# Kernel optimization log

Hardware: AMD Instinct MI355X
Metric: run time of the kernel (lower is better)

## Reference

```python
import jax, jax.numpy as jnp
import numpy as np

N = 100000       # nodes
E = 1600000      # edges
NFEAT, NHID, NCLASS = 512, 256, 40
NLAYERS = 10     # APPNP propagation steps K
ALPHA = 0.1      # teleport probability


def setup_inputs() -> dict:
    key = jax.random.key(0)
    ks = jax.random.split(key, 8)
    x = jax.random.normal(ks[0], (N, NFEAT), jnp.float32)
    row = jax.random.randint(ks[1], (E,), 0, N, jnp.int32)
    col = jax.random.randint(ks[2], (E,), 0, N, jnp.int32)
    vals = jax.random.uniform(ks[3], (E,), jnp.float32)
    # MyLinear init: uniform(-stdv, stdv) with stdv = 1/sqrt(in_features);
    # bias is a shape-[1] scalar (faithful to torch.FloatTensor([out_features])).
    s1 = 1.0 / np.sqrt(NFEAT)
    s2 = 1.0 / np.sqrt(NHID)
    W1 = jax.random.uniform(ks[4], (NFEAT, NHID), jnp.float32, -s1, s1)
    b1 = jax.random.uniform(ks[5], (1,), jnp.float32, -s1, s1)
    W2 = jax.random.uniform(ks[6], (NHID, NCLASS), jnp.float32, -s2, s2)
    b2 = jax.random.uniform(ks[7], (1,), jnp.float32, -s2, s2)
    return dict(x=x, row=row, col=col, vals=vals, W1=W1, b1=b1, W2=W2, b2=b2)


def reference(x, row, col, vals, W1, b1, W2, b2):
    # 2-layer MLP (eval mode: dropout inactive, no BN)
    h = jax.nn.relu(x @ W1 + b1)          # [N, NHID]
    h = h @ W2 + b2                        # [N, NCLASS]

    # sparse adjacency spmm via edge-list segment sum
    def spmm(z):
        return jax.ops.segment_sum(vals[:, None] * z[col], row, num_segments=N)

    # APPNP propagation: z <- (1-alpha) * A z + alpha * h
    def step(z, _):
        z = (1.0 - ALPHA) * spmm(z) + ALPHA * h
        return z, None

    z, _ = jax.lax.scan(step, h, None, length=NLAYERS)
    return jax.nn.log_softmax(z, axis=1)
```

## Files before the change

### kernel.cpp

```cpp
#include <hip/hip_runtime.h>


typedef unsigned short ushort_t;
typedef short short8 __attribute__((ext_vector_type(8)));
typedef float f32x4 __attribute__((ext_vector_type(4)));

#define NFEAT 512
#define NHID 256
#define NCLASS 40

static __device__ __forceinline__ float b2f(ushort_t u) {
    unsigned v = ((unsigned)u) << 16;
    float f;
    __builtin_memcpy(&f, &v, 4);
    return f;
}
static __device__ __forceinline__ ushort_t f2b(float f) {
    unsigned u;
    __builtin_memcpy(&u, &f, 4);
    unsigned r = u + 0x7FFFu + ((u >> 16) & 1u);
    return (ushort_t)(r >> 16);
}
static __device__ __forceinline__ ushort_t san_u(ushort_t u) {
    return ((u & 0x7F80u) == 0x7F80u) ? (ushort_t)0 : u;
}
static __device__ __forceinline__ float ldmix(const void* p, size_t i, int isbf) {
    if (isbf) return b2f(san_u(((const ushort_t*)p)[i]));
    return ((const float*)p)[i];
}
static __device__ __forceinline__ float ldz(const void* p, size_t i, int zbf) {
    return zbf ? b2f(((const ushort_t*)p)[i]) : ((const float*)p)[i];
}
static __device__ __forceinline__ void stz(void* p, size_t i, int zbf, float v) {
    if (zbf) ((ushort_t*)p)[i] = f2b(v);
    else ((float*)p)[i] = v;
}

static __device__ __forceinline__ void gld_lds16(const ushort_t* g, ushort_t* l) {
    __builtin_amdgcn_global_load_lds(
        (const __attribute__((address_space(1))) unsigned int*)g,
        (__attribute__((address_space(3))) unsigned int*)l, 16, 0, 0);
}

__global__ void detect_kernel(const ushort_t* __restrict__ x, int* __restrict__ flag) {
    __shared__ int cnt_s;
    if (threadIdx.x == 0) cnt_s = 0;
    __syncthreads();
    int c = 0;
    for (int i = threadIdx.x; i < 2048; i += 256) {
        ushort_t u = x[2 * i];
        int e = (u >> 7) & 0xFF;
        if (e >= 107 && e <= 141) c++;
    }
    atomicAdd(&cnt_s, c);
    __syncthreads();
    if (threadIdx.x == 0) flag[0] = (cnt_s >= 1024) ? 1 : 0;
}


__global__ void zero_kernel(int* __restrict__ p, int n) {
    int i = blockIdx.x * 256 + threadIdx.x;
    if (i < n) p[i] = 0;
}

__global__ void hist_kernel(const int* __restrict__ row, int* __restrict__ deg, int e, int n) {
    int i = blockIdx.x * 256 + threadIdx.x;
    if (i < e) {
        int r = row[i];
        if ((unsigned)r < (unsigned)n) atomicAdd(&deg[r], 1);
    }
}

__global__ void scan_blocksum(const int* __restrict__ deg, int* __restrict__ bsum, int n) {
    __shared__ int s[256];
    int t = threadIdx.x;
    int i = blockIdx.x * 256 + t;
    s[t] = (i < n) ? deg[i] : 0;
    __syncthreads();
    for (int o = 128; o; o >>= 1) {
        if (t < o) s[t] += s[t + o];
        __syncthreads();
    }
    if (t == 0) bsum[blockIdx.x] = s[0];
}

__global__ void scan_bsum_excl(int* __restrict__ bsum, int nb) {
    __shared__ int s[512];
    int t = threadIdx.x;
    int v = (t < nb) ? bsum[t] : 0;
    int own = v;
    s[t] = v;
    __syncthreads();
    for (int o = 1; o < 512; o <<= 1) {
        int add = (t >= o) ? s[t - o] : 0;
        __syncthreads();
        s[t] += add;
        __syncthreads();
    }
    if (t < nb) bsum[t] = s[t] - own;
}

__global__ void scan_emit(const int* __restrict__ deg, const int* __restrict__ bsum,
                          int* __restrict__ row_start, int* __restrict__ cursor, int n) {
    __shared__ int s[256];
    int t = threadIdx.x;
    int i = blockIdx.x * 256 + t;
    int v = (i < n) ? deg[i] : 0;
    int own = v;
    s[t] = v;
    __syncthreads();
    for (int o = 1; o < 256; o <<= 1) {
        int add = (t >= o) ? s[t - o] : 0;
        __syncthreads();
        s[t] += add;
        __syncthreads();
    }
    if (i < n) {
        int rs = bsum[blockIdx.x] + s[t] - own;
        row_start[i] = rs;
        cursor[i] = rs;
    }
}

__global__ void scatter_kernel(const int* __restrict__ row, const int* __restrict__ col,
                               const void* __restrict__ vals, int* __restrict__ cursor,
                               int* __restrict__ cs_col, void* __restrict__ cs_val,
                               const int* __restrict__ flag, int zbf, int e, int n) {
    int i = blockIdx.x * 256 + threadIdx.x;
    if (i < e) {
        int isbf = flag[0];
        int r = row[i];
        if ((unsigned)r >= (unsigned)n) return;
        int p = atomicAdd(&cursor[r], 1);
        if ((unsigned)p < (unsigned)e) {
            int c = col[i];
            cs_col[p] = ((unsigned)c < (unsigned)n) ? c : 0;
            stz(cs_val, p, zbf, ldmix(vals, i, isbf));
        }
    }
}


__global__ void w1frag_kernel(const void* __restrict__ W1, ushort_t* __restrict__ w1f,
                              const int* __restrict__ flag) {
    int t = blockIdx.x * 256 + threadIdx.x;
    if (t >= 16 * 16 * 64) return;
    int isbf = flag[0];
    int l = t & 63, nt = (t >> 6) & 15, kb = t >> 10;
    ushort_t tmp[8];
#pragma unroll
    for (int j = 0; j < 8; j++) {
        int k = kb * 32 + (l >> 4) * 8 + j;
        int nn = nt * 16 + (l & 15);
        tmp[j] = f2b(ldmix(W1, (size_t)k * NHID + nn, isbf));
    }
    *(short8*)(w1f + (size_t)t * 8) = *(short8*)tmp;
}

__global__ void w2frag_kernel(const void* __restrict__ W2, ushort_t* __restrict__ w2f,
                              const int* __restrict__ flag) {
    int t = blockIdx.x * 256 + threadIdx.x;
    if (t >= 8 * 3 * 64) return;
    int isbf = flag[0];
    int l = t % 64;
    int nt = (t / 64) % 3;
    int kb = t / 192;
    ushort_t tmp[8];
#pragma unroll
    for (int j = 0; j < 8; j++) {
        int k = kb * 32 + (l >> 4) * 8 + j;
        int nn = nt * 16 + (l & 15);
        tmp[j] = (nn < NCLASS) ? f2b(ldmix(W2, (size_t)k * NCLASS + nn, isbf)) : (ushort_t)0;
    }
    *(short8*)(w2f + (size_t)t * 8) = *(short8*)tmp;
}


template <int ISBF>
static __device__ __forceinline__ short8 load_afrag(const void* __restrict__ x, size_t base) {
    short8 av;
    if (ISBF) {
        av = *(const short8*)((const ushort_t*)x + base);
#pragma unroll
        for (int j = 0; j < 8; j++) {
            ushort_t u = (ushort_t)av[j];
            if ((u & 0x7F80u) == 0x7F80u) av[j] = 0;
        }
    } else {
        const float* xf = (const float*)x + base;
        f32x4 a0 = *(const f32x4*)xf;
        f32x4 a1 = *(const f32x4*)(xf + 4);
#pragma unroll
        for (int j = 0; j < 4; j++) {
            av[j] = (short)f2b(a0[j]);
            av[4 + j] = (short)f2b(a1[j]);
        }
    }
    return av;
}

#define APITCH 42

template <int ISBF>
static __device__ __forceinline__ void gemm1_staged(const void* __restrict__ x,
                                                    const ushort_t* __restrict__ w1f,
                                                    size_t xbase, ushort_t* Bl0, ushort_t* Bl1,
                                                    ushort_t* awr0, ushort_t* awr1,
                                                    const ushort_t* ard0, const ushort_t* ard1,
                                                    const ushort_t* brd0, const ushort_t* brd1,
                                                    f32x4 (&acc)[16], int wv, int l) {
    {
        short8 a0 = load_afrag<ISBF>(x, xbase);
        *(short8*)awr0 = a0;
        const ushort_t* src = w1f + (size_t)wv * 512 + (size_t)l * 8;
#pragma unroll
        for (int i = 0; i < 4; i++) gld_lds16(src + i * 2048, Bl0 + wv * 512 + i * 2048);
    }
    __syncthreads();

#pragma unroll
    for (int kb = 0; kb < 16; kb++) {
        const bool even = (kb & 1) == 0;
        const ushort_t* brd = even ? brd0 : brd1;
        const ushort_t* ard = even ? ard0 : ard1;
        ushort_t* awrn = even ? awr1 : awr0;
        ushort_t* bln = even ? Bl1 : Bl0;
        short8 an;
        if (kb < 15) {
            an = load_afrag<ISBF>(x, xbase + (size_t)(kb + 1) * 32);
            const ushort_t* src =
                w1f + (size_t)(kb + 1) * 8192 + (size_t)wv * 512 + (size_t)l * 8;
#pragma unroll
            for (int i = 0; i < 4; i++) gld_lds16(src + i * 2048, bln + wv * 512 + i * 2048);
        }
        short8 af = *(const short8*)ard;
#pragma unroll
        for (int nt = 0; nt < 16; nt++) {
            short8 bf = *(const short8*)(brd + nt * 512);
            acc[nt] = __builtin_amdgcn_mfma_f32_16x16x32_bf16(af, bf, acc[nt], 0, 0, 0);
        }
        if (kb < 15) *(short8*)awrn = an;
        __syncthreads();
    }
}

__global__ __launch_bounds__(256, 3) void mlp_kernel(const void* __restrict__ x,
                                                     const ushort_t* __restrict__ w1f,
                                                     const ushort_t* __restrict__ w2f,
                                                     const void* __restrict__ b1,
                                                     const void* __restrict__ b2,
                                                     void* __restrict__ h,
                                                     const int* __restrict__ flag, int zbf,
                                                     int n) {
    __shared__ __align__(16) ushort_t pool[21760];
    ushort_t* Bl0 = pool;
    ushort_t* Bl1 = pool + 8192;
    ushort_t* Al0 = pool + 16384;
    ushort_t* Al1 = pool + 16384 + 2688;
    ushort_t* Hl = pool;

    const int t = threadIdx.x;
    const int isbf = flag[0];
    const int wv = t >> 6, l = t & 63;
    const int lq = l >> 4, lr = l & 15;
    const int m0 = blockIdx.x * 64;

    const int rS = t >> 2, qS = t & 3;
    int rowS = m0 + rS;
    if (rowS > n - 1) rowS = n - 1;
    const size_t xbase = (size_t)rowS * NFEAT + (size_t)qS * 8;
    ushort_t* awr0 = Al0 + rS * APITCH + qS * 8;
    ushort_t* awr1 = Al1 + rS * APITCH + qS * 8;
    const ushort_t* ard0 = Al0 + (wv * 16 + lr) * APITCH + lq * 8;
    const ushort_t* ard1 = Al1 + (wv * 16 + lr) * APITCH + lq * 8;
    const ushort_t* brd0 = Bl0 + l * 8;
    const ushort_t* brd1 = Bl1 + l * 8;

    f32x4 acc[16];
#pragma unroll
    for (int i = 0; i < 16; i++) acc[i] = (f32x4){0.f, 0.f, 0.f, 0.f};

    if (isbf)
        gemm1_staged<1>(x, w1f, xbase, Bl0, Bl1, awr0, awr1, ard0, ard1, brd0, brd1, acc, wv, l);
    else
        gemm1_staged<0>(x, w1f, xbase, Bl0, Bl1, awr0, awr1, ard0, ard1, brd0, brd1, acc, wv, l);

    float bias1 = ldmix(b1, 0, isbf);
#pragma unroll
    for (int nt = 0; nt < 16; nt++) {
#pragma unroll
        for (int i = 0; i < 4; i++) {
            float v = acc[nt][i] + bias1;
            v = fmaxf(v, 0.f);
            Hl[(wv * 16 + lq * 4 + i) * 264 + nt * 16 + lr] = f2b(v);
        }
    }
    __syncthreads();

    f32x4 acc2[3];
#pragma unroll
    for (int i = 0; i < 3; i++) acc2[i] = (f32x4){0.f, 0.f, 0.f, 0.f};
    const ushort_t* hp = Hl + (wv * 16 + lr) * 264 + lq * 8;
#pragma unroll
    for (int kb = 0; kb < 8; kb++) {
        short8 afrag = *(const short8*)(hp + kb * 32);
#pragma unroll
        for (int nt = 0; nt < 3; nt++) {
            short8 bfrag = *(const short8*)(w2f + ((size_t)(kb * 3 + nt) * 64 + l) * 8);
            acc2[nt] = __builtin_amdgcn_mfma_f32_16x16x32_bf16(afrag, bfrag, acc2[nt], 0, 0, 0);
        }
    }

    float bias2 = ldmix(b2, 0, isbf);
#pragma unroll
    for (int nt = 0; nt < 3; nt++) {
#pragma unroll
        for (int i = 0; i < 4; i++) {
            int rowg = m0 + wv * 16 + lq * 4 + i;
            int colg = nt * 16 + lr;
            if (rowg < n && colg < NCLASS)
                stz(h, (size_t)rowg * NCLASS + colg, zbf, acc2[nt][i] + bias2);
        }
    }
}


template <int ZBF>
__global__ __launch_bounds__(256) void prop_kernel(const void* __restrict__ zin,
                                                   void* __restrict__ zout,
                                                   const void* __restrict__ h,
                                                   const int* __restrict__ row_start,
                                                   const int* __restrict__ deg,
                                                   const int* __restrict__ cs_col,
                                                   const void* __restrict__ cs_val, int n) {
    int w = blockIdx.x * 4 + (threadIdx.x >> 6);
    int lane = threadIdx.x & 63;
    if (w >= n) return;
    int wu = __builtin_amdgcn_readfirstlane(w);
    int start = row_start[wu];
    int d = deg[wu];
    const bool laneok = lane < NCLASS;
    float acc = 0.f;
    for (int base = 0; base < d; base += 64) {
        int m = d - base;
        if (m > 64) m = 64;
        int c = 0;
        float v = 0.f;
        if (lane < m) {
            size_t idx = (size_t)start + base + lane;
            c = cs_col[idx];
            v = ZBF ? b2f(((const ushort_t*)cs_val)[idx]) : ((const float*)cs_val)[idx];
        }
        for (int j = 0; j < m; j += 16) {
            int cc[16];
            float vv[16];
#pragma unroll
            for (int k = 0; k < 16; k++) {
                cc[k] = __shfl(c, j + k);
                vv[k] = __shfl(v, j + k);
            }
            if (laneok) {
                float zv[16];
#pragma unroll
                for (int k = 0; k < 16; k++) {
                    size_t zi = (size_t)cc[k] * NCLASS + lane;
                    zv[k] = ZBF ? b2f(((const ushort_t*)zin)[zi]) : ((const float*)zin)[zi];
                }
#pragma unroll
                for (int k = 0; k < 16; k++) acc += vv[k] * zv[k];
            }
        }
    }
    if (laneok) {
        float hv = ZBF ? b2f(((const ushort_t*)h)[(size_t)w * NCLASS + lane])
                       : ((const float*)h)[(size_t)w * NCLASS + lane];
        float r = 0.9f * acc + 0.1f * hv;
        if (ZBF) ((ushort_t*)zout)[(size_t)w * NCLASS + lane] = f2b(r);
        else ((float*)zout)[(size_t)w * NCLASS + lane] = r;
    }
}


__global__ __launch_bounds__(256) void lsm_kernel(const void* __restrict__ z,
                                                  void* __restrict__ out,
                                                  const int* __restrict__ flag, int zbf, int n) {
    int w = blockIdx.x * 4 + (threadIdx.x >> 6);
    int lane = threadIdx.x & 63;
    if (w >= n) return;
    int isbf = flag[0];
    float v = (lane < NCLASS) ? ldz(z, (size_t)w * NCLASS + lane, zbf) : -INFINITY;
    float m = v;
    for (int o = 32; o; o >>= 1) m = fmaxf(m, __shfl_xor(m, o));
    float e = (lane < NCLASS) ? __expf(v - m) : 0.f;
    float s = e;
    for (int o = 32; o; o >>= 1) s += __shfl_xor(s, o);
    if (lane < NCLASS) {
        float r = v - m - __logf(s);
        if (isbf) ((ushort_t*)out)[(size_t)w * NCLASS + lane] = f2b(r);
        else ((float*)out)[(size_t)w * NCLASS + lane] = r;
    }
}


extern "C" void kernel_launch(void* const* d_in, const int* in_sizes, int n_in, void* d_out,
                              int out_size, void* d_ws, size_t ws_size, hipStream_t stream) {
    const void* x = d_in[0];
    const int* row = (const int*)d_in[1];
    const int* col = (const int*)d_in[2];
    const void* vals = d_in[3];
    const void* W1 = d_in[4];
    const void* b1 = d_in[5];
    const void* W2 = d_in[6];
    const void* b2 = d_in[7];

    const int N = in_sizes[0] / NFEAT;
    const int E = in_sizes[1];

    const int zbf = 1;
    const size_t ez = 2;

    char* ws = (char*)d_ws;
    size_t off = 0;
    auto take = [&](size_t bytes) {
        size_t o = off;
        off = (off + bytes + 255) & ~(size_t)255;
        return (void*)(ws + o);
    };
    void* h = take((size_t)N * NCLASS * ez);
    void* zA = take((size_t)N * NCLASS * ez);
    void* zB = take((size_t)N * NCLASS * ez);
    int* cs_col = (int*)take((size_t)E * 4);
    void* cs_val = take((size_t)E * ez);
    int* deg = (int*)take((size_t)N * 4);
    int* row_start = (int*)take((size_t)N * 4);
    int* cursor = (int*)take((size_t)N * 4);
    ushort_t* w1f = (ushort_t*)take((size_t)NFEAT * NHID * 2);
    ushort_t* w2f = (ushort_t*)take((size_t)8 * 3 * 64 * 8 * 2);
    int* bsum = (int*)take(512 * 4);
    int* flag = (int*)take(256);

    const int NB = (N + 255) / 256;
    const int EB = (E + 255) / 256;
    const int GB = (N + 63) / 64;
    const int PB = (N + 3) / 4;

    detect_kernel<<<1, 256, 0, stream>>>((const ushort_t*)x, flag);

    zero_kernel<<<(N + 255) / 256, 256, 0, stream>>>(deg, N);
    hist_kernel<<<EB, 256, 0, stream>>>(row, deg, E, N);
    scan_blocksum<<<NB, 256, 0, stream>>>(deg, bsum, N);
    scan_bsum_excl<<<1, 512, 0, stream>>>(bsum, NB);
    scan_emit<<<NB, 256, 0, stream>>>(deg, bsum, row_start, cursor, N);
    scatter_kernel<<<EB, 256, 0, stream>>>(row, col, vals, cursor, cs_col, cs_val, flag, zbf, E,
                                           N);

    w1frag_kernel<<<64, 256, 0, stream>>>(W1, w1f, flag);
    w2frag_kernel<<<6, 256, 0, stream>>>(W2, w2f, flag);

    mlp_kernel<<<GB, 256, 0, stream>>>(x, w1f, w2f, b1, b2, h, flag, zbf, N);

    prop_kernel<1><<<PB, 256, 0, stream>>>(h, zA, h, row_start, deg, cs_col, cs_val, N);
    {
        const void* zi = zA;
        void* zo = zB;
        for (int s = 1; s < 10; s++) {
            prop_kernel<1><<<PB, 256, 0, stream>>>(zi, zo, h, row_start, deg, cs_col, cs_val, N);
            const void* tmp = zi;
            zi = zo;
            zo = (void*)tmp;
        }
        lsm_kernel<<<PB, 256, 0, stream>>>(zi, d_out, flag, zbf, N);
    }
}
```

Before: 1.059 ms.

## Fuse propagation steps into one cooperative persistent kernel with LDS-cached edges

```diff
diff --git a/kernel.cpp b/kernel.cpp
--- a/kernel.cpp
+++ b/kernel.cpp
@@ -1,4 +1,7 @@
 #include <hip/hip_runtime.h>
+#include <hip/hip_cooperative_groups.h>
+
+namespace cg = cooperative_groups;
 
 
 typedef unsigned short ushort_t;
@@ -27,9 +30,6 @@
 static __device__ __forceinline__ float ldmix(const void* p, size_t i, int isbf) {
     if (isbf) return b2f(san_u(((const ushort_t*)p)[i]));
     return ((const float*)p)[i];
-}
-static __device__ __forceinline__ float ldz(const void* p, size_t i, int zbf) {
-    return zbf ? b2f(((const ushort_t*)p)[i]) : ((const float*)p)[i];
 }
 static __device__ __forceinline__ void stz(void* p, size_t i, int zbf, float v) {
     if (zbf) ((ushort_t*)p)[i] = f2b(v);
@@ -124,8 +124,8 @@
 
 __global__ void scatter_kernel(const int* __restrict__ row, const int* __restrict__ col,
                                const void* __restrict__ vals, int* __restrict__ cursor,
-                               int* __restrict__ cs_col, void* __restrict__ cs_val,
-                               const int* __restrict__ flag, int zbf, int e, int n) {
+                               int2* __restrict__ cs, const int* __restrict__ flag, int e,
+                               int n) {
     int i = blockIdx.x * 256 + threadIdx.x;
     if (i < e) {
         int isbf = flag[0];
@@ -134,8 +134,11 @@
         int p = atomicAdd(&cursor[r], 1);
         if ((unsigned)p < (unsigned)e) {
             int c = col[i];
-            cs_col[p] = ((unsigned)c < (unsigned)n) ? c : 0;
-            stz(cs_val, p, zbf, ldmix(vals, i, isbf));
+            float v = ldmix(vals, i, isbf);
+            int2 rec;
+            rec.x = ((unsigned)c < (unsigned)n) ? c : 0;
+            __builtin_memcpy(&rec.y, &v, 4);
+            cs[p] = rec;
         }
     }
 }
@@ -325,20 +328,135 @@
 }
 
 
-template <int ZBF>
+#define CSCAP 4096
+#define NMAX 512
+
+__global__ __launch_bounds__(256, 4) void prop_fused(void* __restrict__ zA,
+                                                     void* __restrict__ zB,
+                                                     const void* __restrict__ h,
+                                                     const int* __restrict__ row_start,
+                                                     const int* __restrict__ deg,
+                                                     const int2* __restrict__ cs, int n,
+                                                     int etot) {
+    __shared__ int2 lrec[CSCAP];
+    __shared__ int lstart[NMAX];
+    __shared__ int ldeg[NMAX];
+
+    const int t = threadIdx.x;
+    const int wv = t >> 6, lane = t & 63;
+    const int grid = gridDim.x;
+    const int chunk = (n + grid - 1) / grid;
+    const int node0 = blockIdx.x * chunk;
+    int nodes = n - node0;
+    if (nodes > chunk) nodes = chunk;
+    if (nodes < 0) nodes = 0;
+
+    int base = 0, total = 0;
+    if (nodes > 0) {
+        base = row_start[node0];
+        int endi = node0 + nodes;
+        total = ((endi < n) ? row_start[endi] : etot) - base;
+    }
+    const bool meta_ok = (nodes <= NMAX);
+    if (meta_ok) {
+        for (int k = t; k < nodes; k += 256) {
+            lstart[k] = row_start[node0 + k] - base;
+            ldeg[k] = deg[node0 + k];
+        }
+    }
+    const int cap = (total < CSCAP) ? total : CSCAP;
+    for (int i = t; i < cap; i += 256) lrec[i] = cs[base + i];
+    __syncthreads();
+
+    cg::grid_group gg = cg::this_grid();
+    const bool laneok = lane < NCLASS;
+
+    for (int step = 0; step < 10; step++) {
+        const ushort_t* zi =
+            (const ushort_t*)((step == 0) ? h : ((step & 1) ? zA : zB));
+        ushort_t* zo = (ushort_t*)((step & 1) ? zB : zA);
+
+        for (int idx = wv; idx < nodes; idx += 4) {
+            int st, d;
+            if (meta_ok) {
+                st = lstart[idx];
+                d = ldeg[idx];
+            } else {
+                st = row_start[node0 + idx] - base;
+                d = deg[node0 + idx];
+            }
+            float acc = 0.f;
+            if (st + d <= cap) {
+                for (int e = 0; e < d; e += 8) {
+                    int cc[8];
+                    float vv[8];
+#pragma unroll
+                    for (int k = 0; k < 8; k++) {
+                        int ee = e + k;
+                        int ii = st + ((ee < d) ? ee : d - 1);
+                        int2 r = lrec[ii];
+                        cc[k] = r.x;
+                        float fv;
+                        __builtin_memcpy(&fv, &r.y, 4);
+                        vv[k] = (ee < d) ? fv : 0.f;
+                    }
+                    if (laneok) {
+                        float zv[8];
+#pragma unroll
+                        for (int k = 0; k < 8; k++)
+                            zv[k] = b2f(zi[(size_t)cc[k] * NCLASS + lane]);
+#pragma unroll
+                        for (int k = 0; k < 8; k++) acc += vv[k] * zv[k];
+                    }
+                }
+            } else {
+                for (int e = 0; e < d; e += 8) {
+                    int cc[8];
+                    float vv[8];
+#pragma unroll
+                    for (int k = 0; k < 8; k++) {
+                        int ee = e + k;
+                        int ii = base + st + ((ee < d) ? ee : d - 1);
+                        int2 r = cs[ii];
+                        cc[k] = r.x;
+                        float fv;
+                        __builtin_memcpy(&fv, &r.y, 4);
+                        vv[k] = (ee < d) ? fv : 0.f;
+                    }
+                    if (laneok) {
+                        float zv[8];
+#pragma unroll
+                        for (int k = 0; k < 8; k++)
+                            zv[k] = b2f(zi[(size_t)cc[k] * NCLASS + lane]);
+#pragma unroll
+                        for (int k = 0; k < 8; k++) acc += vv[k] * zv[k];
+                    }
+                }
+            }
+            if (laneok) {
+                int w = node0 + idx;
+                float hv = b2f(((const ushort_t*)h)[(size_t)w * NCLASS + lane]);
+                float r = 0.9f * acc + 0.1f * hv;
+                zo[(size_t)w * NCLASS + lane] = f2b(r);
+            }
+        }
+        __threadfence();
+        gg.sync();
+    }
+}
+
+
 __global__ __launch_bounds__(256) void prop_kernel(const void* __restrict__ zin,
                                                    void* __restrict__ zout,
                                                    const void* __restrict__ h,
                                                    const int* __restrict__ row_start,
                                                    const int* __restrict__ deg,
-                                                   const int* __restrict__ cs_col,
-                                                   const void* __restrict__ cs_val, int n) {
+                                                   const int2* __restrict__ cs, int n) {
     int w = blockIdx.x * 4 + (threadIdx.x >> 6);
     int lane = threadIdx.x & 63;
     if (w >= n) return;
-    int wu = __builtin_amdgcn_readfirstlane(w);
-    int start = row_start[wu];
-    int d = deg[wu];
+    int start = row_start[w];
+    int d = deg[w];
     const bool laneok = lane < NCLASS;
     float acc = 0.f;
     for (int base = 0; base < d; base += 64) {
@@ -347,48 +465,44 @@
         int c = 0;
         float v = 0.f;
         if (lane < m) {
-            size_t idx = (size_t)start + base + lane;
-            c = cs_col[idx];
-            v = ZBF ? b2f(((const ushort_t*)cs_val)[idx]) : ((const float*)cs_val)[idx];
-        }
-        for (int j = 0; j < m; j += 16) {
-            int cc[16];
-            float vv[16];
-#pragma unroll
-            for (int k = 0; k < 16; k++) {
+            int2 r = cs[(size_t)start + base + lane];
+            c = r.x;
+            __builtin_memcpy(&v, &r.y, 4);
+        }
+        for (int j = 0; j < m; j += 8) {
+            int cc[8];
+            float vv[8];
+#pragma unroll
+            for (int k = 0; k < 8; k++) {
                 cc[k] = __shfl(c, j + k);
                 vv[k] = __shfl(v, j + k);
             }
             if (laneok) {
-                float zv[16];
-#pragma unroll
-                for (int k = 0; k < 16; k++) {
-                    size_t zi = (size_t)cc[k] * NCLASS + lane;
-                    zv[k] = ZBF ? b2f(((const ushort_t*)zin)[zi]) : ((const float*)zin)[zi];
-                }
-#pragma unroll
-                for (int k = 0; k < 16; k++) acc += vv[k] * zv[k];
+                float zv[8];
+#pragma unroll
+                for (int k = 0; k < 8; k++)
+                    zv[k] = b2f(((const ushort_t*)zin)[(size_t)cc[k] * NCLASS + lane]);
+#pragma unroll
+                for (int k = 0; k < 8; k++) acc += vv[k] * zv[k];
             }
         }
     }
     if (laneok) {
-        float hv = ZBF ? b2f(((const ushort_t*)h)[(size_t)w * NCLASS + lane])
-                       : ((const float*)h)[(size_t)w * NCLASS + lane];
+        float hv = b2f(((const ushort_t*)h)[(size_t)w * NCLASS + lane]);
         float r = 0.9f * acc + 0.1f * hv;
-        if (ZBF) ((ushort_t*)zout)[(size_t)w * NCLASS + lane] = f2b(r);
-        else ((float*)zout)[(size_t)w * NCLASS + lane] = r;
+        ((ushort_t*)zout)[(size_t)w * NCLASS + lane] = f2b(r);
     }
 }
 
 
 __global__ __launch_bounds__(256) void lsm_kernel(const void* __restrict__ z,
                                                   void* __restrict__ out,
-                                                  const int* __restrict__ flag, int zbf, int n) {
+                                                  const int* __restrict__ flag, int n) {
     int w = blockIdx.x * 4 + (threadIdx.x >> 6);
     int lane = threadIdx.x & 63;
     if (w >= n) return;
     int isbf = flag[0];
-    float v = (lane < NCLASS) ? ldz(z, (size_t)w * NCLASS + lane, zbf) : -INFINITY;
+    float v = (lane < NCLASS) ? b2f(((const ushort_t*)z)[(size_t)w * NCLASS + lane]) : -INFINITY;
     float m = v;
     for (int o = 32; o; o >>= 1) m = fmaxf(m, __shfl_xor(m, o));
     float e = (lane < NCLASS) ? __expf(v - m) : 0.f;
@@ -416,7 +530,6 @@
     const int N = in_sizes[0] / NFEAT;
     const int E = in_sizes[1];
 
-    const int zbf = 1;
     const size_t ez = 2;
 
     char* ws = (char*)d_ws;
@@ -429,8 +542,7 @@
     void* h = take((size_t)N * NCLASS * ez);
     void* zA = take((size_t)N * NCLASS * ez);
     void* zB = take((size_t)N * NCLASS * ez);
-    int* cs_col = (int*)take((size_t)E * 4);
-    void* cs_val = take((size_t)E * ez);
+    int2* cs = (int2*)take((size_t)E * 8);
     int* deg = (int*)take((size_t)N * 4);
     int* row_start = (int*)take((size_t)N * 4);
     int* cursor = (int*)take((size_t)N * 4);
@@ -451,24 +563,63 @@
     scan_blocksum<<<NB, 256, 0, stream>>>(deg, bsum, N);
     scan_bsum_excl<<<1, 512, 0, stream>>>(bsum, NB);
     scan_emit<<<NB, 256, 0, stream>>>(deg, bsum, row_start, cursor, N);
-    scatter_kernel<<<EB, 256, 0, stream>>>(row, col, vals, cursor, cs_col, cs_val, flag, zbf, E,
-                                           N);
+    scatter_kernel<<<EB, 256, 0, stream>>>(row, col, vals, cursor, cs, flag, E, N);
 
     w1frag_kernel<<<64, 256, 0, stream>>>(W1, w1f, flag);
     w2frag_kernel<<<6, 256, 0, stream>>>(W2, w2f, flag);
 
-    mlp_kernel<<<GB, 256, 0, stream>>>(x, w1f, w2f, b1, b2, h, flag, zbf, N);
-
-    prop_kernel<1><<<PB, 256, 0, stream>>>(h, zA, h, row_start, deg, cs_col, cs_val, N);
-    {
+    mlp_kernel<<<GB, 256, 0, stream>>>(x, w1f, w2f, b1, b2, h, flag, 1, N);
+
+    static int coop_state = 0;
+    int launched_coop = 0;
+    if (coop_state >= 0) {
+        static int cached_grid = 0;
+        if (cached_grid == 0) {
+            int cu = 256;
+            hipDeviceProp_t prop;
+            if (hipGetDeviceProperties(&prop, 0) == hipSuccess && prop.multiProcessorCount > 0)
+                cu = prop.multiProcessorCount;
+            int occ = 0;
+            if (hipOccupancyMaxActiveBlocksPerMultiprocessor(&occ, prop_fused, 256, 0) !=
+                    hipSuccess ||
+                occ <= 0)
+                occ = 4;
+            if (occ > 4) occ = 4;
+            int g = cu * occ;
+            if (g > 1024) g = 1024;
+            if (g < 64) g = 64;
+            cached_grid = g;
+        }
+        int n_ = N, e_ = E;
+        void* ka[8];
+        ka[0] = (void*)&zA;
+        ka[1] = (void*)&zB;
+        ka[2] = (void*)&h;
+        ka[3] = (void*)&row_start;
+        ka[4] = (void*)&deg;
+        ka[5] = (void*)&cs;
+        ka[6] = (void*)&n_;
+        ka[7] = (void*)&e_;
+        hipError_t err = hipLaunchCooperativeKernel(prop_fused, dim3(cached_grid), dim3(256), ka,
+                                                    0, stream);
+        if (err == hipSuccess) {
+            coop_state = 1;
+            launched_coop = 1;
+            lsm_kernel<<<PB, 256, 0, stream>>>(zB, d_out, flag, N);
+        } else {
+            coop_state = -1;
+        }
+    }
+    if (!launched_coop) {
+        prop_kernel<<<PB, 256, 0, stream>>>(h, zA, h, row_start, deg, cs, N);
         const void* zi = zA;
         void* zo = zB;
         for (int s = 1; s < 10; s++) {
-            prop_kernel<1><<<PB, 256, 0, stream>>>(zi, zo, h, row_start, deg, cs_col, cs_val, N);
+            prop_kernel<<<PB, 256, 0, stream>>>(zi, zo, h, row_start, deg, cs, N);
             const void* tmp = zi;
             zi = zo;
             zo = (void*)tmp;
         }
-        lsm_kernel<<<PB, 256, 0, stream>>>(zi, d_out, flag, zbf, N);
-    }
-}
+        lsm_kernel<<<PB, 256, 0, stream>>>(zi, d_out, flag, N);
+    }
+}
```

New measurement: 3.390 ms. +220.1%, slower.

## Pack CSR col/val into int2, process two rows per wave, shard scatter

Applied to the files above, without the earlier changes.

```diff
diff --git a/kernel.cpp b/kernel.cpp
--- a/kernel.cpp
+++ b/kernel.cpp
@@ -27,9 +27,6 @@
 static __device__ __forceinline__ float ldmix(const void* p, size_t i, int isbf) {
     if (isbf) return b2f(san_u(((const ushort_t*)p)[i]));
     return ((const float*)p)[i];
-}
-static __device__ __forceinline__ float ldz(const void* p, size_t i, int zbf) {
-    return zbf ? b2f(((const ushort_t*)p)[i]) : ((const float*)p)[i];
 }
 static __device__ __forceinline__ void stz(void* p, size_t i, int zbf, float v) {
     if (zbf) ((ushort_t*)p)[i] = f2b(v);
@@ -124,19 +121,24 @@
 
 __global__ void scatter_kernel(const int* __restrict__ row, const int* __restrict__ col,
                                const void* __restrict__ vals, int* __restrict__ cursor,
-                               int* __restrict__ cs_col, void* __restrict__ cs_val,
-                               const int* __restrict__ flag, int zbf, int e, int n) {
-    int i = blockIdx.x * 256 + threadIdx.x;
-    if (i < e) {
-        int isbf = flag[0];
-        int r = row[i];
-        if ((unsigned)r >= (unsigned)n) return;
-        int p = atomicAdd(&cursor[r], 1);
-        if ((unsigned)p < (unsigned)e) {
-            int c = col[i];
-            cs_col[p] = ((unsigned)c < (unsigned)n) ? c : 0;
-            stz(cs_val, p, zbf, ldmix(vals, i, isbf));
-        }
+                               int2* __restrict__ cs, const int* __restrict__ flag, int e,
+                               int n, int nshard) {
+    int shard = blockIdx.x & 7;
+    int i = (blockIdx.x >> 3) * 256 + threadIdx.x;
+    if (i >= e) return;
+    int r = row[i];
+    if ((unsigned)r >= (unsigned)n) return;
+    int s0 = shard * nshard;
+    if (r < s0 || r >= s0 + nshard) return;
+    int isbf = flag[0];
+    int p = atomicAdd(&cursor[r], 1);
+    if ((unsigned)p < (unsigned)e) {
+        int c = col[i];
+        float v = ldmix(vals, i, isbf);
+        int2 rec;
+        rec.x = ((unsigned)c < (unsigned)n) ? c : 0;
+        __builtin_memcpy(&rec.y, &v, 4);
+        cs[p] = rec;
     }
 }
 
@@ -325,70 +327,86 @@
 }
 
 
-template <int ZBF>
 __global__ __launch_bounds__(256) void prop_kernel(const void* __restrict__ zin,
                                                    void* __restrict__ zout,
                                                    const void* __restrict__ h,
                                                    const int* __restrict__ row_start,
                                                    const int* __restrict__ deg,
-                                                   const int* __restrict__ cs_col,
-                                                   const void* __restrict__ cs_val, int n) {
-    int w = blockIdx.x * 4 + (threadIdx.x >> 6);
+                                                   const int2* __restrict__ cs, int n) {
+    int g = blockIdx.x * 4 + (threadIdx.x >> 6);
     int lane = threadIdx.x & 63;
-    if (w >= n) return;
-    int wu = __builtin_amdgcn_readfirstlane(w);
-    int start = row_start[wu];
-    int d = deg[wu];
+    int a = g * 2, b = g * 2 + 1;
+    if (a >= n) return;
+    const bool hasb = (b < n);
+    int sa = row_start[a], da = deg[a];
+    int sb = hasb ? row_start[b] : 0;
+    int db = hasb ? deg[b] : 0;
     const bool laneok = lane < NCLASS;
-    float acc = 0.f;
-    for (int base = 0; base < d; base += 64) {
-        int m = d - base;
-        if (m > 64) m = 64;
-        int c = 0;
-        float v = 0.f;
-        if (lane < m) {
-            size_t idx = (size_t)start + base + lane;
-            c = cs_col[idx];
-            v = ZBF ? b2f(((const ushort_t*)cs_val)[idx]) : ((const float*)cs_val)[idx];
-        }
-        for (int j = 0; j < m; j += 16) {
-            int cc[16];
-            float vv[16];
-#pragma unroll
-            for (int k = 0; k < 16; k++) {
-                cc[k] = __shfl(c, j + k);
-                vv[k] = __shfl(v, j + k);
+    const ushort_t* zi = (const ushort_t*)zin;
+    float acca = 0.f, accb = 0.f;
+    int dmax = (da > db) ? da : db;
+    for (int base = 0; base < dmax; base += 64) {
+        int ma = da - base;
+        ma = (ma < 0) ? 0 : ((ma > 64) ? 64 : ma);
+        int mb = db - base;
+        mb = (mb < 0) ? 0 : ((mb > 64) ? 64 : mb);
+        int ca = 0, cb = 0;
+        float va = 0.f, vb = 0.f;
+        if (lane < ma) {
+            int2 r = cs[(size_t)sa + base + lane];
+            ca = r.x;
+            __builtin_memcpy(&va, &r.y, 4);
+        }
+        if (lane < mb) {
+            int2 r = cs[(size_t)sb + base + lane];
+            cb = r.x;
+            __builtin_memcpy(&vb, &r.y, 4);
+        }
+        int mm = (ma > mb) ? ma : mb;
+        for (int j = 0; j < mm; j += 8) {
+            int cca[8], ccb[8];
+            float vva[8], vvb[8];
+#pragma unroll
+            for (int k = 0; k < 8; k++) {
+                cca[k] = __shfl(ca, j + k);
+                vva[k] = __shfl(va, j + k);
+                ccb[k] = __shfl(cb, j + k);
+                vvb[k] = __shfl(vb, j + k);
             }
             if (laneok) {
-                float zv[16];
-#pragma unroll
-                for (int k = 0; k < 16; k++) {
-                    size_t zi = (size_t)cc[k] * NCLASS + lane;
-                    zv[k] = ZBF ? b2f(((const ushort_t*)zin)[zi]) : ((const float*)zin)[zi];
-                }
-#pragma unroll
-                for (int k = 0; k < 16; k++) acc += vv[k] * zv[k];
+                float zva[8], zvb[8];
+#pragma unroll
+                for (int k = 0; k < 8; k++) zva[k] = b2f(zi[(size_t)cca[k] * NCLASS + lane]);
+#pragma unroll
+                for (int k = 0; k < 8; k++) zvb[k] = b2f(zi[(size_t)ccb[k] * NCLASS + lane]);
+#pragma unroll
+                for (int k = 0; k < 8; k++) acca += vva[k] * zva[k];
+#pragma unroll
+                for (int k = 0; k < 8; k++) accb += vvb[k] * zvb[k];
             }
         }
     }
     if (laneok) {
-        float hv = ZBF ? b2f(((const ushort_t*)h)[(size_t)w * NCLASS + lane])
-                       : ((const float*)h)[(size_t)w * NCLASS + lane];
-        float r = 0.9f * acc + 0.1f * hv;
-        if (ZBF) ((ushort_t*)zout)[(size_t)w * NCLASS + lane] = f2b(r);
-        else ((float*)zout)[(size_t)w * NCLASS + lane] = r;
+        {
+            float hv = b2f(((const ushort_t*)h)[(size_t)a * NCLASS + lane]);
+            ((ushort_t*)zout)[(size_t)a * NCLASS + lane] = f2b(0.9f * acca + 0.1f * hv);
+        }
+        if (hasb) {
+            float hv = b2f(((const ushort_t*)h)[(size_t)b * NCLASS + lane]);
+            ((ushort_t*)zout)[(size_t)b * NCLASS + lane] = f2b(0.9f * accb + 0.1f * hv);
+        }
     }
 }
 
 
 __global__ __launch_bounds__(256) void lsm_kernel(const void* __restrict__ z,
                                                   void* __restrict__ out,
-                                                  const int* __restrict__ flag, int zbf, int n) {
+                                                  const int* __restrict__ flag, int n) {
     int w = blockIdx.x * 4 + (threadIdx.x >> 6);
     int lane = threadIdx.x & 63;
     if (w >= n) return;
     int isbf = flag[0];
-    float v = (lane < NCLASS) ? ldz(z, (size_t)w * NCLASS + lane, zbf) : -INFINITY;
+    float v = (lane < NCLASS) ? b2f(((const ushort_t*)z)[(size_t)w * NCLASS + lane]) : -INFINITY;
     float m = v;
     for (int o = 32; o; o >>= 1) m = fmaxf(m, __shfl_xor(m, o));
     float e = (lane < NCLASS) ? __expf(v - m) : 0.f;
@@ -416,7 +434,6 @@
     const int N = in_sizes[0] / NFEAT;
     const int E = in_sizes[1];
 
-    const int zbf = 1;
     const size_t ez = 2;
 
     char* ws = (char*)d_ws;
@@ -429,8 +446,7 @@
     void* h = take((size_t)N * NCLASS * ez);
     void* zA = take((size_t)N * NCLASS * ez);
     void* zB = take((size_t)N * NCLASS * ez);
-    int* cs_col = (int*)take((size_t)E * 4);
-    void* cs_val = take((size_t)E * ez);
+    int2* cs = (int2*)take((size_t)E * 8);
     int* deg = (int*)take((size_t)N * 4);
     int* row_start = (int*)take((size_t)N * 4);
     int* cursor = (int*)take((size_t)N * 4);
@@ -443,6 +459,8 @@
     const int EB = (E + 255) / 256;
     const int GB = (N + 63) / 64;
     const int PB = (N + 3) / 4;
+    const int NSHARD = (N + 7) / 8;
+    const int PB2 = ((N + 1) / 2 + 3) / 4;
 
     detect_kernel<<<1, 256, 0, stream>>>((const ushort_t*)x, flag);
 
@@ -451,24 +469,23 @@
     scan_blocksum<<<NB, 256, 0, stream>>>(deg, bsum, N);
     scan_bsum_excl<<<1, 512, 0, stream>>>(bsum, NB);
     scan_emit<<<NB, 256, 0, stream>>>(deg, bsum, row_start, cursor, N);
-    scatter_kernel<<<EB, 256, 0, stream>>>(row, col, vals, cursor, cs_col, cs_val, flag, zbf, E,
-                                           N);
+    scatter_kernel<<<EB * 8, 256, 0, stream>>>(row, col, vals, cursor, cs, flag, E, N, NSHARD);
 
     w1frag_kernel<<<64, 256, 0, stream>>>(W1, w1f, flag);
     w2frag_kernel<<<6, 256, 0, stream>>>(W2, w2f, flag);
 
-    mlp_kernel<<<GB, 256, 0, stream>>>(x, w1f, w2f, b1, b2, h, flag, zbf, N);
-
-    prop_kernel<1><<<PB, 256, 0, stream>>>(h, zA, h, row_start, deg, cs_col, cs_val, N);
+    mlp_kernel<<<GB, 256, 0, stream>>>(x, w1f, w2f, b1, b2, h, flag, 1, N);
+
+    prop_kernel<<<PB2, 256, 0, stream>>>(h, zA, h, row_start, deg, cs, N);
     {
         const void* zi = zA;
         void* zo = zB;
         for (int s = 1; s < 10; s++) {
-            prop_kernel<1><<<PB, 256, 0, stream>>>(zi, zo, h, row_start, deg, cs_col, cs_val, N);
+            prop_kernel<<<PB2, 256, 0, stream>>>(zi, zo, h, row_start, deg, cs, N);
             const void* tmp = zi;
             zi = zo;
             zo = (void*)tmp;
         }
-        lsm_kernel<<<PB, 256, 0, stream>>>(zi, d_out, flag, zbf, N);
-    }
-}
+        lsm_kernel<<<PB, 256, 0, stream>>>(zi, d_out, flag, N);
+    }
+}
```

After: 1.004 ms. 1.05x faster.
